# Kernel optimization log

Measured on AMD Instinct MI355X. Metric: run time of the kernel, lower is better.

## Reference

```python
import jax, jax.numpy as jnp
import numpy as np

H = 16      # num_heads
D = 64      # head_dim
BQ = 64     # block_size_q
BKV = 64    # block_size_kv


def setup_inputs() -> dict:
    key = jax.random.key(0)
    ks = jax.random.split(key, 5)
    B, S, dim = 2, 2048, 1024
    x = jax.random.normal(ks[0], (B, S, dim), dtype=jnp.float32)
    Wq = jax.random.normal(ks[1], (dim, H * D), dtype=jnp.float32) * 0.02
    Wk = jax.random.normal(ks[2], (dim, H * D), dtype=jnp.float32) * 0.02
    Wv = jax.random.normal(ks[3], (dim, H * D), dtype=jnp.float32) * 0.02
    Wo = jax.random.normal(ks[4], (H * D, dim), dtype=jnp.float32) * 0.02
    return {"x": x, "Wq": Wq, "Wk": Wk, "Wv": Wv, "Wo": Wo}


def _flash_tiled(q, k, v, scale):
    # q,k,v: (B, H, S, D). Non-causal tiled attention with online softmax,
    # faithfully replicating the source's per-iteration division by l_new.
    B, nh, S, d = q.shape
    nq, nkv = S // BQ, S // BKV
    qb = q.reshape(B, nh, nq, BQ, d)                       # all q blocks at once (outer loop vectorized)
    kb = k.reshape(B, nh, nkv, BKV, d).transpose(2, 0, 1, 3, 4)  # (nkv, B, H, BKV, D)
    vb = v.reshape(B, nh, nkv, BKV, d).transpose(2, 0, 1, 3, 4)

    o0 = jnp.zeros((B, nh, nq, BQ, d), q.dtype)
    m0 = jnp.full((B, nh, nq, BQ), -jnp.inf, q.dtype)
    l0 = jnp.zeros((B, nh, nq, BQ), q.dtype)

    def step(carry, kv):
        o, m, l = carry
        kj, vj = kv
        s = jnp.einsum('bhnqd,bhkd->bhnqk', qb, kj) * scale   # (B,H,nq,BQ,BKV)
        m_new = jnp.maximum(m, s.max(axis=-1))
        p = jnp.exp(s - m_new[..., None])
        alpha = jnp.exp(m - m_new)
        l_new = alpha * l + p.sum(axis=-1)
        # NOTE: division by l_new every iteration, as in the source module.
        o_new = (alpha[..., None] * o + jnp.einsum('bhnqk,bhkd->bhnqd', p, vj)) / l_new[..., None]
        return (o_new, m_new, l_new), None

    (o, _, _), _ = jax.lax.scan(step, (o0, m0, l0), (kb, vb))
    return o.reshape(B, nh, S, d)


def reference(x, Wq, Wk, Wv, Wo):
    B, S, dim = x.shape
    scale = D ** -0.5
    q = (x @ Wq).reshape(B, S, H, D).transpose(0, 2, 1, 3)
    k = (x @ Wk).reshape(B, S, H, D).transpose(0, 2, 1, 3)
    v = (x @ Wv).reshape(B, S, H, D).transpose(0, 2, 1, 3)
    o = _flash_tiled(q, k, v, scale)                       # (B,H,S,D)
    out = o.transpose(0, 2, 1, 3).reshape(B, S, H * D)
    return out @ Wo
```

## Files before the change

### kernel.cpp

```cpp
#include <hip/hip_runtime.h>
#include <hip/hip_bf16.h>
#include <math.h>

#define BB   2
#define SS   2048
#define DIM  1024
#define NH   16
#define HD   64
#define MTOT (BB * SS)

typedef unsigned short ushortT;
typedef __attribute__((ext_vector_type(8))) short short8v;
typedef __attribute__((ext_vector_type(4))) float float4v;
typedef __attribute__((ext_vector_type(16))) float float16v;

union FragU { short8v v; unsigned short us[8]; unsigned int u[4]; };

__device__ inline unsigned short f2bf(float x) {
    unsigned u = __builtin_bit_cast(unsigned, x);
    u += 0x7fffu + ((u >> 16) & 1u);
    return (unsigned short)(u >> 16);
}
__device__ inline float bf2f(unsigned short h) {
    unsigned u = ((unsigned)h) << 16;
    return __builtin_bit_cast(float, u);
}
__device__ inline void split_tr(float x, unsigned short& hi, unsigned short& lo) {
    unsigned u = __builtin_bit_cast(unsigned, x);
    hi = (unsigned short)(u >> 16);
    float hf = __builtin_bit_cast(float, u & 0xffff0000u);
    lo = (unsigned short)(__builtin_bit_cast(unsigned, x - hf) >> 16);
}
__device__ inline void split4(const float4& x, short4& hi, short4& lo) {
    unsigned short h0 = f2bf(x.x), h1 = f2bf(x.y), h2 = f2bf(x.z), h3 = f2bf(x.w);
    hi = make_short4((short)h0, (short)h1, (short)h2, (short)h3);
    lo = make_short4((short)f2bf(x.x - bf2f(h0)), (short)f2bf(x.y - bf2f(h1)),
                     (short)f2bf(x.z - bf2f(h2)), (short)f2bf(x.w - bf2f(h3)));
}
__device__ inline void gld_lds16(const void* g, void* l) {
    __builtin_amdgcn_global_load_lds(
        (const __attribute__((address_space(1))) void*)g,
        (__attribute__((address_space(3))) void*)l, 16, 0, 0);
}
__device__ inline unsigned cvt_pk_bf16(float a, float b) {
    unsigned r;
    asm("v_cvt_pk_bf16_f32 %0, %1, %2" : "=v"(r) : "v"(a), "v"(b));
    return r;
}
__device__ inline void permlane32_swap(unsigned &a, unsigned &b) {
    asm("v_permlane32_swap_b32 %0, %1" : "+v"(a), "+v"(b));
}

__global__ __launch_bounds__(256) void convert_split_kernel(
    const float* __restrict__ in, ushortT* __restrict__ hi, ushortT* __restrict__ lo, int n4)
{
    int t = blockIdx.x * 256 + threadIdx.x;
    if (t < n4) {
        float4 x = ((const float4*)in)[t];
        short4 h, l; split4(x, h, l);
        ((short4*)hi)[t] = h;
        ((short4*)lo)[t] = l;
    }
}

__global__ __launch_bounds__(256) void transpose_split_kernel(
    const float* __restrict__ W0, const float* __restrict__ W1,
    const float* __restrict__ W2, const float* __restrict__ W3,
    ushortT* __restrict__ WtH, ushortT* __restrict__ WtL)
{
    const int z = blockIdx.z;
    const float* __restrict__ W = (z == 0) ? W0 : (z == 1) ? W1 : (z == 2) ? W2 : W3;
    ushortT* H = WtH + (size_t)z * 1024 * 1024;
    ushortT* L = WtL + (size_t)z * 1024 * 1024;

    __shared__ float T[64][65];
    const int k0 = blockIdx.y * 64, n0 = blockIdx.x * 64;
    const int tid = threadIdx.x;
    const int c4 = (tid & 15) * 4;

#pragma unroll
    for (int i = 0; i < 4; i++) {
        int r = (tid >> 4) + 16 * i;
        *(float4*)&T[r][c4] = *(const float4*)(W + (size_t)(k0 + r) * 1024 + n0 + c4);
    }
    __syncthreads();
#pragma unroll
    for (int i = 0; i < 4; i++) {
        int n = (tid >> 4) + 16 * i;
        float4 vv = make_float4(T[c4 + 0][n], T[c4 + 1][n], T[c4 + 2][n], T[c4 + 3][n]);
        short4 h, l; split4(vv, h, l);
        *(short4*)&H[(size_t)(n0 + n) * 1024 + k0 + c4] = h;
        *(short4*)&L[(size_t)(n0 + n) * 1024 + k0 + c4] = l;
    }
}

__global__ __launch_bounds__(256) void kv_convert_kernel(
    const float* __restrict__ kw,
    ushortT* __restrict__ KhG, ushortT* __restrict__ KlG)
{
    const int jb = blockIdx.x, bh = blockIdx.y;
    const int b = bh >> 4, h = bh & 15;

    __shared__ float T[64][68];
    const int tid = threadIdx.x;
    const size_t ibase = (size_t)b * SS * DIM + (size_t)h * HD + (size_t)(jb * 64) * DIM;
    const int c4 = (tid & 15) * 4;
#pragma unroll
    for (int i = 0; i < 4; i++) {
        int r = (tid >> 4) + 16 * i;
        *(float4*)&T[r][c4] = *(const float4*)(kw + ibase + (size_t)r * DIM + c4);
    }
    __syncthreads();

    ushortT* oh = KhG + (size_t)(bh * 32 + jb) * 4096;
    ushortT* ol = KlG + (size_t)(bh * 32 + jb) * 4096;

#pragma unroll
    for (int i = 0; i < 2; i++) {
        const int s = tid + i * 256;
        const int f = s >> 6;
        const int lane = s & 63;
        const int ds = f >> 1, kvt = f & 1;
        const int kv = kvt * 32 + (lane & 31);
        const int d0 = ds * 16 + (lane >> 5) * 8;
        ushortT hv[8], lv[8];
#pragma unroll
        for (int j = 0; j < 8; j++) split_tr(T[kv][d0 + j], hv[j], lv[j]);
        *(short4*)&oh[s * 8]     = *(short4*)&hv[0];
        *(short4*)&oh[s * 8 + 4] = *(short4*)&hv[4];
        *(short4*)&ol[s * 8]     = *(short4*)&lv[0];
        *(short4*)&ol[s * 8 + 4] = *(short4*)&lv[4];
    }
}

__global__ __launch_bounds__(256, 2) void gemm_bt_split_kernel(
    const ushortT* __restrict__ Ah, const ushortT* __restrict__ Al,
    const ushortT* __restrict__ BtH, const ushortT* __restrict__ BtL,
    float* __restrict__ Y0, float* __restrict__ Y1,
    ushortT* __restrict__ VhG, ushortT* __restrict__ VlG)
{
    const int z = blockIdx.z;
    const ushortT* __restrict__ Bh = BtH + (size_t)z * 1024 * 1024;
    const ushortT* __restrict__ Bl = BtL + (size_t)z * 1024 * 1024;

    const int K = 1024, N = 1024;
    const int m0 = blockIdx.y * 128;
    const int n0 = blockIdx.x * 128;

    __shared__ __align__(16) ushortT AhS[128 * 32];
    __shared__ __align__(16) ushortT AlS[128 * 32];
    __shared__ __align__(16) ushortT BhS[128 * 32];
    __shared__ __align__(16) ushortT BlS[128 * 32];

    const int tid  = threadIdx.x;
    const int wave = tid >> 6, lane = tid & 63;
    const int quad = lane >> 4, l15 = lane & 15;
    const int wm = wave >> 1, wn = wave & 1;

    const int s0 = tid, s1 = tid + 256;
    const int ar0 = s0 >> 2, ak0 = (s0 & 3) * 8;
    const int ar1 = s1 >> 2, ak1 = (s1 & 3) * 8;

    float4v acc[4][4];
#pragma unroll
    for (int i = 0; i < 4; i++)
#pragma unroll
        for (int j = 0; j < 4; j++) acc[i][j] = (float4v){0.f, 0.f, 0.f, 0.f};

    for (int k0 = 0; k0 < K; k0 += 32) {
        __syncthreads();
        gld_lds16(Ah + (size_t)(m0 + ar0) * K + k0 + ak0, &AhS[s0 * 8]);
        gld_lds16(Ah + (size_t)(m0 + ar1) * K + k0 + ak1, &AhS[s1 * 8]);
        gld_lds16(Al + (size_t)(m0 + ar0) * K + k0 + ak0, &AlS[s0 * 8]);
        gld_lds16(Al + (size_t)(m0 + ar1) * K + k0 + ak1, &AlS[s1 * 8]);
        gld_lds16(Bh + (size_t)(n0 + ar0) * K + k0 + ak0, &BhS[s0 * 8]);
        gld_lds16(Bh + (size_t)(n0 + ar1) * K + k0 + ak1, &BhS[s1 * 8]);
        gld_lds16(Bl + (size_t)(n0 + ar0) * K + k0 + ak0, &BlS[s0 * 8]);
        gld_lds16(Bl + (size_t)(n0 + ar1) * K + k0 + ak1, &BlS[s1 * 8]);
        __syncthreads();

        FragU ah[4], al[4], bh[4], bl[4];
#pragma unroll
        for (int t = 0; t < 4; t++) {
            ah[t].v = *(const short8v*)&AhS[(wm * 64 + t * 16 + l15) * 32 + quad * 8];
            al[t].v = *(const short8v*)&AlS[(wm * 64 + t * 16 + l15) * 32 + quad * 8];
            bh[t].v = *(const short8v*)&BhS[(wn * 64 + t * 16 + l15) * 32 + quad * 8];
            bl[t].v = *(const short8v*)&BlS[(wn * 64 + t * 16 + l15) * 32 + quad * 8];
        }
#pragma unroll
        for (int mt = 0; mt < 4; mt++)
#pragma unroll
            for (int nt = 0; nt < 4; nt++) {
                acc[mt][nt] = __builtin_amdgcn_mfma_f32_16x16x32_bf16(ah[mt].v, bh[nt].v, acc[mt][nt], 0, 0, 0);
                acc[mt][nt] = __builtin_amdgcn_mfma_f32_16x16x32_bf16(ah[mt].v, bl[nt].v, acc[mt][nt], 0, 0, 0);
                acc[mt][nt] = __builtin_amdgcn_mfma_f32_16x16x32_bf16(al[mt].v, bh[nt].v, acc[mt][nt], 0, 0, 0);
            }
    }

    if (z == 2) {
        const int b  = m0 >> 11;
        const int jb = ((m0 & 2047) >> 6) + wm;
        const int h  = (n0 >> 6) + wn;
        const size_t tb = (size_t)((b * 16 + h) * 32 + jb) * 4096;
        ushortT* vh = VhG + tb;
        ushortT* vl = VlG + tb;
#pragma unroll
        for (int mt = 0; mt < 4; mt++)
#pragma unroll
            for (int nt = 0; nt < 4; nt++) {
                const int off = ((((nt >> 1) * 4 + mt) * 64 +
                                  (quad >> 1) * 32 + (nt & 1) * 16 + l15) * 8) +
                                (quad & 1) * 4;
                float4 vv = make_float4(acc[mt][nt][0], acc[mt][nt][1],
                                        acc[mt][nt][2], acc[mt][nt][3]);
                unsigned short h0, l0, h1, l1, h2, l2, h3, l3;
                split_tr(vv.x, h0, l0); split_tr(vv.y, h1, l1);
                split_tr(vv.z, h2, l2); split_tr(vv.w, h3, l3);
                *(short4*)&vh[off] = make_short4((short)h0, (short)h1, (short)h2, (short)h3);
                *(short4*)&vl[off] = make_short4((short)l0, (short)l1, (short)l2, (short)l3);
            }
    } else {
        float* __restrict__ Y = (z == 0) ? Y0 : Y1;
#pragma unroll
        for (int mt = 0; mt < 4; mt++)
#pragma unroll
            for (int r = 0; r < 4; r++) {
                const int row = m0 + wm * 64 + mt * 16 + quad * 4 + r;
                float* yp = Y + (size_t)row * N + n0 + wn * 64 + l15;
#pragma unroll
                for (int nt = 0; nt < 4; nt++)
                    yp[nt * 16] = acc[mt][nt][r];
            }
    }
}

__global__ __launch_bounds__(256, 2) void attn_mfma_kernel(
    const float* __restrict__ q,
    const ushortT* __restrict__ KhG, const ushortT* __restrict__ KlG,
    const ushortT* __restrict__ VhG, const ushortT* __restrict__ VlG,
    ushortT* __restrict__ Oh, ushortT* __restrict__ Ol)
{
    __shared__ __align__(16) ushortT SMEM[32768];

    const int tid  = threadIdx.x;
    const int wave = tid >> 6, lane = tid & 63;
    const int l31 = lane & 31, hi5 = lane >> 5;
    const int bh = blockIdx.y, b = bh >> 4, h = bh & 15;
    const size_t base = (size_t)b * SS * DIM + (size_t)h * HD;
    const int qs0 = blockIdx.x * 128 + wave * 32;
    const int lane8 = lane * 8;
    const int sl0 = wave * 128 + lane, sl1 = sl0 + 64;

    const float qscale = 0.125f * 1.4426950408889634f;
    FragU Qh[4], Ql[4];
    {
        const int qrow = qs0 + l31;
#pragma unroll
        for (int ds = 0; ds < 4; ds++) {
            const float* p0 = q + base + (size_t)qrow * DIM + ds * 16 + hi5 * 8;
            float4 a = *(const float4*)(p0);
            float4 c = *(const float4*)(p0 + 4);
            float e[8] = {a.x, a.y, a.z, a.w, c.x, c.y, c.z, c.w};
#pragma unroll
            for (int j = 0; j < 8; j++) {
                float x = e[j] * qscale;
                unsigned short hs = f2bf(x);
                Qh[ds].us[j] = hs;
                Ql[ds].us[j] = f2bf(x - bf2f(hs));
            }
        }
    }

    float16v Oacc[2];
#pragma unroll
    for (int dt = 0; dt < 2; dt++)
        Oacc[dt] = (float16v){0.f,0.f,0.f,0.f,0.f,0.f,0.f,0.f,
                              0.f,0.f,0.f,0.f,0.f,0.f,0.f,0.f};

    float m_run = -INFINITY;
    float l_run = 0.f;

    auto stage = [&](int bbuf, int jb) {
        const size_t tb = (size_t)(bh * 32 + jb) * 4096;
        ushortT* S = SMEM + bbuf * 16384;
        gld_lds16(KhG + tb + sl0 * 8, &S[sl0 * 8]);
        gld_lds16(KhG + tb + sl1 * 8, &S[sl1 * 8]);
        gld_lds16(KlG + tb + sl0 * 8, &S[4096 + sl0 * 8]);
        gld_lds16(KlG + tb + sl1 * 8, &S[4096 + sl1 * 8]);
        gld_lds16(VhG + tb + sl0 * 8, &S[8192 + sl0 * 8]);
        gld_lds16(VhG + tb + sl1 * 8, &S[8192 + sl1 * 8]);
        gld_lds16(VlG + tb + sl0 * 8, &S[12288 + sl0 * 8]);
        gld_lds16(VlG + tb + sl1 * 8, &S[12288 + sl1 * 8]);
    };

    stage(0, 0);
    __syncthreads();
    int bb = 0;

    for (int jb = 0; jb < 32; jb++) {
        if (jb < 31) stage(bb ^ 1, jb + 1);

        const ushortT* KhS = SMEM + bb * 16384;
        const ushortT* KlS = KhS + 4096;
        const ushortT* VhS = KhS + 8192;
        const ushortT* VlS = KhS + 12288;

        float16v st[2];
#pragma unroll
        for (int t = 0; t < 2; t++)
            st[t] = (float16v){0.f,0.f,0.f,0.f,0.f,0.f,0.f,0.f,
                               0.f,0.f,0.f,0.f,0.f,0.f,0.f,0.f};

#pragma unroll
        for (int ds = 0; ds < 4; ds++) {
            FragU kh0, kl0, kh1, kl1;
            kh0.v = *(const short8v*)&KhS[(ds * 2 + 0) * 512 + lane8];
            kl0.v = *(const short8v*)&KlS[(ds * 2 + 0) * 512 + lane8];
            kh1.v = *(const short8v*)&KhS[(ds * 2 + 1) * 512 + lane8];
            kl1.v = *(const short8v*)&KlS[(ds * 2 + 1) * 512 + lane8];
            st[0] = __builtin_amdgcn_mfma_f32_32x32x16_bf16(kh0.v, Qh[ds].v, st[0], 0, 0, 0);
            st[0] = __builtin_amdgcn_mfma_f32_32x32x16_bf16(kh0.v, Ql[ds].v, st[0], 0, 0, 0);
            st[0] = __builtin_amdgcn_mfma_f32_32x32x16_bf16(kl0.v, Qh[ds].v, st[0], 0, 0, 0);
            st[1] = __builtin_amdgcn_mfma_f32_32x32x16_bf16(kh1.v, Qh[ds].v, st[1], 0, 0, 0);
            st[1] = __builtin_amdgcn_mfma_f32_32x32x16_bf16(kh1.v, Ql[ds].v, st[1], 0, 0, 0);
            st[1] = __builtin_amdgcn_mfma_f32_32x32x16_bf16(kl1.v, Qh[ds].v, st[1], 0, 0, 0);
        }

        float oscale, inv;
        {
            float g[8];
#pragma unroll
            for (int t = 0; t < 2; t++)
#pragma unroll
                for (int i = 0; i < 4; i++)
                    g[t * 4 + i] = fmaxf(fmaxf(st[t][4 * i], st[t][4 * i + 1]),
                                         fmaxf(st[t][4 * i + 2], st[t][4 * i + 3]));
            float vmax = fmaxf(fmaxf(fmaxf(g[0], g[1]), fmaxf(g[2], g[3])),
                               fmaxf(fmaxf(g[4], g[5]), fmaxf(g[6], g[7])));
            vmax = fmaxf(vmax, __shfl_xor(vmax, 32, 64));
            const float mn = fmaxf(m_run, vmax);
            const float al = __builtin_amdgcn_exp2f(m_run - mn);

            float ssum = 0.f;
#pragma unroll
            for (int t = 0; t < 2; t++)
#pragma unroll
                for (int r = 0; r < 16; r++) {
                    const float p = __builtin_amdgcn_exp2f(st[t][r] - mn);
                    st[t][r] = p;
                    ssum += p;
                }
            ssum += __shfl_xor(ssum, 32, 64);
            const float ln = al * l_run + ssum;
            inv = __builtin_amdgcn_rcpf(ln);
            oscale = al * inv;
#pragma unroll
            for (int t = 0; t < 2; t++)
#pragma unroll
                for (int r = 0; r < 16; r++)
                    st[t][r] *= inv;
            m_run = mn;
            l_run = ln;
        }

#pragma unroll
        for (int dt = 0; dt < 2; dt++)
#pragma unroll
            for (int r = 0; r < 16; r++)
                Oacc[dt][r] *= oscale;

#pragma unroll
        for (int kvs = 0; kvs < 4; kvs++) {
            const int kvt = kvs >> 1;
            const int R = (kvs & 1) * 8;
            float p0 = st[kvt][R + 0], p1 = st[kvt][R + 1];
            float p2 = st[kvt][R + 2], p3 = st[kvt][R + 3];
            float p4 = st[kvt][R + 4], p5 = st[kvt][R + 5];
            float p6 = st[kvt][R + 6], p7 = st[kvt][R + 7];
            unsigned X0 = cvt_pk_bf16(p0, p1), X1 = cvt_pk_bf16(p2, p3);
            unsigned Y0 = cvt_pk_bf16(p4, p5), Y1 = cvt_pk_bf16(p6, p7);
            float e0 = p0 - __builtin_bit_cast(float, X0 << 16);
            float e1 = p1 - __builtin_bit_cast(float, X0 & 0xffff0000u);
            float e2 = p2 - __builtin_bit_cast(float, X1 << 16);
            float e3 = p3 - __builtin_bit_cast(float, X1 & 0xffff0000u);
            float e4 = p4 - __builtin_bit_cast(float, Y0 << 16);
            float e5 = p5 - __builtin_bit_cast(float, Y0 & 0xffff0000u);
            float e6 = p6 - __builtin_bit_cast(float, Y1 << 16);
            float e7 = p7 - __builtin_bit_cast(float, Y1 & 0xffff0000u);
            unsigned Z0 = cvt_pk_bf16(e0, e1), Z1 = cvt_pk_bf16(e2, e3);
            unsigned W0 = cvt_pk_bf16(e4, e5), W1 = cvt_pk_bf16(e6, e7);
            permlane32_swap(X0, Y0);
            permlane32_swap(X1, Y1);
            permlane32_swap(Z0, W0);
            permlane32_swap(Z1, W1);
            FragU Phf, Plf;
            Phf.u[0] = X0; Phf.u[1] = X1; Phf.u[2] = Y0; Phf.u[3] = Y1;
            Plf.u[0] = Z0; Plf.u[1] = Z1; Plf.u[2] = W0; Plf.u[3] = W1;

#pragma unroll
            for (int dt = 0; dt < 2; dt++) {
                FragU vh, vl;
                vh.v = *(const short8v*)&VhS[(dt * 4 + kvs) * 512 + lane8];
                vl.v = *(const short8v*)&VlS[(dt * 4 + kvs) * 512 + lane8];
                Oacc[dt] = __builtin_amdgcn_mfma_f32_32x32x16_bf16(vh.v, Phf.v, Oacc[dt], 0, 0, 0);
                Oacc[dt] = __builtin_amdgcn_mfma_f32_32x32x16_bf16(vl.v, Phf.v, Oacc[dt], 0, 0, 0);
                Oacc[dt] = __builtin_amdgcn_mfma_f32_32x32x16_bf16(vh.v, Plf.v, Oacc[dt], 0, 0, 0);
            }
        }

        __syncthreads();
        bb ^= 1;
    }

    float* EP = ((float*)SMEM) + wave * 1056;
    const int qq = lane >> 1, dh = (lane & 1) * 16;
#pragma unroll
    for (int dt = 0; dt < 2; dt++) {
#pragma unroll
        for (int g = 0; g < 4; g++) {
            float4 wv = make_float4(Oacc[dt][4 * g + 0], Oacc[dt][4 * g + 1],
                                    Oacc[dt][4 * g + 2], Oacc[dt][4 * g + 3]);
            *(float4*)&EP[l31 * 33 + g * 8 + hi5 * 4] = wv;
        }
        float vals[16];
#pragma unroll
        for (int k4 = 0; k4 < 4; k4++)
            *(float4*)&vals[k4 * 4] = *(const float4*)&EP[qq * 33 + dh + k4 * 4];

        unsigned ho[8], lo8[8];
#pragma unroll
        for (int kk = 0; kk < 8; kk++) {
            unsigned short h0, l0, h1, l1;
            split_tr(vals[2 * kk], h0, l0);
            split_tr(vals[2 * kk + 1], h1, l1);
            ho[kk]  = (unsigned)h0 | ((unsigned)h1 << 16);
            lo8[kk] = (unsigned)l0 | ((unsigned)l1 << 16);
        }
        const int qrow = qs0 + qq;
        const size_t off = (size_t)(b * SS + qrow) * DIM + h * HD + dt * 32 + dh;
        *(uint4*)&Oh[off]     = make_uint4(ho[0], ho[1], ho[2], ho[3]);
        *(uint4*)&Oh[off + 8] = make_uint4(ho[4], ho[5], ho[6], ho[7]);
        *(uint4*)&Ol[off]     = make_uint4(lo8[0], lo8[1], lo8[2], lo8[3]);
        *(uint4*)&Ol[off + 8] = make_uint4(lo8[4], lo8[5], lo8[6], lo8[7]);
    }
}

extern "C" void kernel_launch(void* const* d_in, const int* in_sizes, int n_in,
                              void* d_out, int out_size, void* d_ws, size_t ws_size,
                              hipStream_t stream)
{
    const float* x  = (const float*)d_in[0];
    const float* Wq = (const float*)d_in[1];
    const float* Wk = (const float*)d_in[2];
    const float* Wv = (const float*)d_in[3];
    const float* Wo = (const float*)d_in[4];
    float* out = (float*)d_out;

    char* w = (char*)d_ws;
    float*   qw  = (float*)(w);
    float*   kw  = (float*)(w + ((size_t)16 << 20));
    ushortT* VhG = (ushortT*)(w + ((size_t)32 << 20));
    ushortT* VlG = (ushortT*)(w + ((size_t)40 << 20));
    ushortT* XhS = (ushortT*)(w + ((size_t)48 << 20));
    ushortT* XlS = (ushortT*)(w + ((size_t)56 << 20));
    ushortT* WtH = (ushortT*)(w + ((size_t)64 << 20));
    ushortT* WtL = (ushortT*)(w + ((size_t)72 << 20));
    ushortT* KhG = (ushortT*)(w + ((size_t)80 << 20));
    ushortT* KlG = (ushortT*)(w + ((size_t)88 << 20));
    ushortT* OhS = (ushortT*)kw;
    ushortT* OlS = (ushortT*)(w + ((size_t)24 << 20));

    dim3 blk(256);
    const int n4 = MTOT * DIM / 4;

    convert_split_kernel<<<dim3(n4 / 256), blk, 0, stream>>>(x, XhS, XlS, n4);
    transpose_split_kernel<<<dim3(16, 16, 4), blk, 0, stream>>>(Wq, Wk, Wv, Wo, WtH, WtL);

    gemm_bt_split_kernel<<<dim3(8, 32, 3), blk, 0, stream>>>(
        XhS, XlS, WtH, WtL, qw, kw, VhG, VlG);

    kv_convert_kernel<<<dim3(32, 32), blk, 0, stream>>>(kw, KhG, KlG);

    attn_mfma_kernel<<<dim3(16, 32), blk, 0, stream>>>(qw, KhG, KlG, VhG, VlG, OhS, OlS);

    gemm_bt_split_kernel<<<dim3(8, 32, 1), blk, 0, stream>>>(
        OhS, OlS, WtH + (size_t)3 * 1024 * 1024, WtL + (size_t)3 * 1024 * 1024,
        out, nullptr, nullptr, nullptr);
}
```

Measured before the change: 326.3 us.

## Software-pipeline QK of next tile with softmax/PV of current tile

Splits K and V staging into separate double buffers, prefetching K two tiles ahead and V one tile ahead. Each iteration computes the QK^T scores for the next KV tile before doing softmax and PV on the current one, so MFMA work can overlap the exp/reduction phase. The loop is manually unrolled by two to alternate score registers and buffers. This raises register pressure from the second score accumulator and relies on one barrier per iteration to order buffer reuse.

```diff
diff --git a/kernel.cpp b/kernel.cpp
--- a/kernel.cpp
+++ b/kernel.cpp
@@ -251,6 +251,11 @@
     const int lane8 = lane * 8;
     const int sl0 = wave * 128 + lane, sl1 = sl0 + 64;
 
+    ushortT* K0 = SMEM;
+    ushortT* K1 = SMEM + 8192;
+    ushortT* V0 = SMEM + 16384;
+    ushortT* V1 = SMEM + 24576;
+
     const float qscale = 0.125f * 1.4426950408889634f;
     FragU Qh[4], Ql[4];
     {
@@ -280,37 +285,28 @@
     float m_run = -INFINITY;
     float l_run = 0.f;
 
-    auto stage = [&](int bbuf, int jb) {
-        const size_t tb = (size_t)(bh * 32 + jb) * 4096;
-        ushortT* S = SMEM + bbuf * 16384;
-        gld_lds16(KhG + tb + sl0 * 8, &S[sl0 * 8]);
-        gld_lds16(KhG + tb + sl1 * 8, &S[sl1 * 8]);
-        gld_lds16(KlG + tb + sl0 * 8, &S[4096 + sl0 * 8]);
-        gld_lds16(KlG + tb + sl1 * 8, &S[4096 + sl1 * 8]);
-        gld_lds16(VhG + tb + sl0 * 8, &S[8192 + sl0 * 8]);
-        gld_lds16(VhG + tb + sl1 * 8, &S[8192 + sl1 * 8]);
-        gld_lds16(VlG + tb + sl0 * 8, &S[12288 + sl0 * 8]);
-        gld_lds16(VlG + tb + sl1 * 8, &S[12288 + sl1 * 8]);
+    auto stage_K = [&](int t, ushortT* dst) {
+        const size_t tb = (size_t)(bh * 32 + t) * 4096;
+        gld_lds16(KhG + tb + sl0 * 8, &dst[sl0 * 8]);
+        gld_lds16(KhG + tb + sl1 * 8, &dst[sl1 * 8]);
+        gld_lds16(KlG + tb + sl0 * 8, &dst[4096 + sl0 * 8]);
+        gld_lds16(KlG + tb + sl1 * 8, &dst[4096 + sl1 * 8]);
     };
-
-    stage(0, 0);
-    __syncthreads();
-    int bb = 0;
-
-    for (int jb = 0; jb < 32; jb++) {
-        if (jb < 31) stage(bb ^ 1, jb + 1);
-
-        const ushortT* KhS = SMEM + bb * 16384;
-        const ushortT* KlS = KhS + 4096;
-        const ushortT* VhS = KhS + 8192;
-        const ushortT* VlS = KhS + 12288;
-
-        float16v st[2];
+    auto stage_V = [&](int t, ushortT* dst) {
+        const size_t tb = (size_t)(bh * 32 + t) * 4096;
+        gld_lds16(VhG + tb + sl0 * 8, &dst[sl0 * 8]);
+        gld_lds16(VhG + tb + sl1 * 8, &dst[sl1 * 8]);
+        gld_lds16(VlG + tb + sl0 * 8, &dst[4096 + sl0 * 8]);
+        gld_lds16(VlG + tb + sl1 * 8, &dst[4096 + sl1 * 8]);
+    };
+
+    auto qk = [&](const ushortT* Kb, float16v (&st)[2]) {
+        const ushortT* KhS = Kb;
+        const ushortT* KlS = Kb + 4096;
 #pragma unroll
         for (int t = 0; t < 2; t++)
             st[t] = (float16v){0.f,0.f,0.f,0.f,0.f,0.f,0.f,0.f,
                                0.f,0.f,0.f,0.f,0.f,0.f,0.f,0.f};
-
 #pragma unroll
         for (int ds = 0; ds < 4; ds++) {
             FragU kh0, kl0, kh1, kl1;
@@ -325,7 +321,11 @@
             st[1] = __builtin_amdgcn_mfma_f32_32x32x16_bf16(kh1.v, Ql[ds].v, st[1], 0, 0, 0);
             st[1] = __builtin_amdgcn_mfma_f32_32x32x16_bf16(kl1.v, Qh[ds].v, st[1], 0, 0, 0);
         }
-
+    };
+
+    auto finish = [&](float16v (&st)[2], const ushortT* Vb) {
+        const ushortT* VhS = Vb;
+        const ushortT* VlS = Vb + 4096;
         float oscale, inv;
         {
             float g[8];
@@ -407,9 +407,29 @@
                 Oacc[dt] = __builtin_amdgcn_mfma_f32_32x32x16_bf16(vh.v, Plf.v, Oacc[dt], 0, 0, 0);
             }
         }
-
+    };
+
+    float16v stA[2], stB[2];
+
+    stage_K(0, K0);
+    stage_K(1, K1);
+    stage_V(0, V0);
+    __syncthreads();
+    qk(K0, stA);
+    __syncthreads();
+
+    auto iter = [&](int jb, float16v (&SC)[2], float16v (&SN)[2],
+                    ushortT* Kc, ushortT* Kn, ushortT* Vc, ushortT* Vn) {
+        if (jb <= 29) stage_K(jb + 2, Kc);
+        if (jb <= 30) stage_V(jb + 1, Vn);
+        if (jb <= 30) qk(Kn, SN);
+        finish(SC, Vc);
         __syncthreads();
-        bb ^= 1;
+    };
+
+    for (int jb = 0; jb < 32; jb += 2) {
+        iter(jb,     stA, stB, K0, K1, V0, V1);
+        iter(jb + 1, stB, stA, K1, K0, V1, V0);
     }
 
     float* EP = ((float*)SMEM) + wave * 1056;
```

Measured after the change: 319.4 us. 2.1% less time.
